# Optimization experiments

Hardware: AMD Instinct MI355X
Metric: run time of the kernel (lower is better)

## Reference

```python
import jax, jax.numpy as jnp
import numpy as np

N_HEAD = 16
HEAD_DIM = 64

def rotate_half(x):
    x1, x2 = jnp.split(x, 2, axis=-1)
    return jnp.concatenate((-x2, x1), axis=-1)

def rope_tables(T, dim):
    inv_freq = 1.0 / (10000.0 ** (jnp.arange(0, dim, 2, dtype=jnp.float32) / dim))
    t = jnp.arange(T, dtype=jnp.float32)
    freqs = jnp.einsum('i,j->ij', t, inv_freq)          # [T, dim/2]
    emb = jnp.concatenate((freqs, freqs), axis=-1)       # [T, dim]
    return jnp.cos(emb)[None, None], jnp.sin(emb)[None, None]  # [1,1,T,dim]

def setup_inputs() -> dict:
    key = jax.random.key(0)
    k1, k2, k3 = jax.random.split(key, 3)
    C = N_HEAD * HEAD_DIM
    x = jax.random.normal(k1, (2, 2048, C), dtype=jnp.float32)
    W_qkv = jax.random.normal(k2, (C, 3 * C), dtype=jnp.float32) * (1.0 / np.sqrt(C))
    W_proj = jax.random.normal(k3, (C, C), dtype=jnp.float32) * (1.0 / np.sqrt(C))
    return {"x": x, "W_qkv": W_qkv, "W_proj": W_proj}

def reference(x, W_qkv, W_proj):
    B, T, C = x.shape
    qkv = x @ W_qkv                                       # [B,T,3C]
    q, k, v = jnp.split(qkv, 3, axis=-1)
    def to_heads(a):
        return a.reshape(B, T, N_HEAD, HEAD_DIM).transpose(0, 2, 1, 3)  # [B,H,T,D]
    q, k, v = to_heads(q), to_heads(k), to_heads(v)
    cos, sin = rope_tables(T, HEAD_DIM)
    q = q * cos + rotate_half(q) * sin
    k = k * cos + rotate_half(k) * sin
    scale = 1.0 / jnp.sqrt(jnp.asarray(HEAD_DIM, dtype=x.dtype))
    scores = jnp.einsum('bhqd,bhkd->bhqk', q, k) * scale  # [B,H,T,T]
    causal = jnp.tril(jnp.ones((T, T), dtype=bool))
    scores = jnp.where(causal[None, None], scores, jnp.finfo(scores.dtype).min)
    attn = jax.nn.softmax(scores, axis=-1)
    out = jnp.einsum('bhqk,bhkd->bhqd', attn, v)          # [B,H,T,D]
    out = out.transpose(0, 2, 1, 3).reshape(B, T, C)
    return out @ W_proj
```

## Files before the change

### kernel.cpp

```cpp
#include <hip/hip_runtime.h>
#include <cstdint>
#include <cstddef>

typedef __attribute__((ext_vector_type(8))) short bf16x8;
typedef __attribute__((ext_vector_type(4))) float f32x4;

__device__ __forceinline__ unsigned short f2bf(float f) {
  unsigned int u = __builtin_bit_cast(unsigned int, f);
  u += 0x7FFFu + ((u >> 16) & 1u);
  return (unsigned short)(u >> 16);
}
__device__ __forceinline__ float bf2f(unsigned short h) {
  unsigned int u = ((unsigned int)h) << 16;
  return __builtin_bit_cast(float, u);
}

__device__ __forceinline__ void gl_lds16(const unsigned short* g, unsigned short* l) {
  __builtin_amdgcn_global_load_lds(
      (const __attribute__((address_space(1))) unsigned int*)(uintptr_t)g,
      (__attribute__((address_space(3))) unsigned int*)(unsigned int)(uintptr_t)l,
      16, 0, 0);
}

__global__ void k_prep(const float* __restrict__ x,
                       const float* __restrict__ Wqkv,
                       const float* __restrict__ Wproj,
                       unsigned short* __restrict__ xb,
                       unsigned short* __restrict__ wqt,
                       unsigned short* __restrict__ wpt,
                       float2* __restrict__ cstab) {
  __shared__ float tile[32][33];
  const int bid = blockIdx.x, tid = threadIdx.x;
  if (bid < 4096) {
    int i = bid * 256 + tid;
    float4 v = reinterpret_cast<const float4*>(x)[i];
    uint2 o;
    o.x = (unsigned int)f2bf(v.x) | ((unsigned int)f2bf(v.y) << 16);
    o.y = (unsigned int)f2bf(v.z) | ((unsigned int)f2bf(v.w) << 16);
    reinterpret_cast<uint2*>(xb)[i] = o;
  } else if (bid < 8192) {
    const float* in; unsigned short* out; int rows, cols, bx, by;
    if (bid < 7168) { in = Wqkv; out = wqt; rows = 1024; cols = 3072; bx = (bid - 4096) % 96; by = (bid - 4096) / 96; }
    else            { in = Wproj; out = wpt; rows = 1024; cols = 1024; bx = (bid - 7168) % 32; by = (bid - 7168) / 32; }
    int c0 = bx * 32, r0 = by * 32;
    int tx = tid & 31, ty = tid >> 5;
#pragma unroll
    for (int j = 0; j < 4; j++)
      tile[ty + j * 8][tx] = in[(size_t)(r0 + ty + j * 8) * cols + c0 + tx];
    __syncthreads();
#pragma unroll
    for (int j = 0; j < 4; j++)
      out[(size_t)(c0 + ty + j * 8) * rows + r0 + tx] = f2bf(tile[tx][ty + j * 8]);
  } else {
    int i = (bid - 8192) * 256 + tid;
    int t = i >> 5, j = i & 31;
    float invf = __powf(10000.0f, -(float)j / 32.0f);
    float ang = (float)t * invf;
    cstab[i] = make_float2(cosf(ang), sinf(ang));
  }
}

__global__ void k_gemm_qkv(const unsigned short* __restrict__ A,
                           const unsigned short* __restrict__ Bt,
                           const float2* __restrict__ cstab,
                           unsigned short* __restrict__ qh,
                           unsigned short* __restrict__ kh,
                           unsigned short* __restrict__ vt) {
  const int K = 1024;
  __shared__ unsigned short Ta[128 * 32];
  __shared__ unsigned short Tb[128 * 32];
  const int tid = threadIdx.x;
  const int bid0 = blockIdx.y * 24 + blockIdx.x;
  const int bid = (bid0 & 7) * 96 + (bid0 >> 3);
  const int m0 = (bid / 24) * 128, n0 = (bid % 24) * 128;
  const int w = tid >> 6, l = tid & 63;
  const int lr = l & 15, lg = l >> 4;
  const int wm = (w >> 1) * 64, wn = (w & 1) * 64;
  const int ssr = w * 32 + (l >> 2);
  const int ssc = (l & 3) * 8;
  unsigned short* ta0 = &Ta[w * 1024];
  unsigned short* tb0 = &Tb[w * 1024];
  f32x4 acc[4][4] = {};
  for (int k0 = 0; k0 < K; k0 += 32) {
    __syncthreads();
    gl_lds16(&A[(size_t)(m0 + ssr) * K + k0 + ssc],       ta0);
    gl_lds16(&A[(size_t)(m0 + ssr + 16) * K + k0 + ssc],  ta0 + 512);
    gl_lds16(&Bt[(size_t)(n0 + ssr) * K + k0 + ssc],      tb0);
    gl_lds16(&Bt[(size_t)(n0 + ssr + 16) * K + k0 + ssc], tb0 + 512);
    __syncthreads();
    bf16x8 af[4], bfr[4];
#pragma unroll
    for (int i = 0; i < 4; i++)
      af[i] = *(const bf16x8*)&Ta[(wm + i * 16 + lr) * 32 + lg * 8];
#pragma unroll
    for (int j = 0; j < 4; j++)
      bfr[j] = *(const bf16x8*)&Tb[(wn + j * 16 + lr) * 32 + lg * 8];
#pragma unroll
    for (int i = 0; i < 4; i++)
#pragma unroll
      for (int j = 0; j < 4; j++)
        acc[i][j] = __builtin_amdgcn_mfma_f32_16x16x32_bf16(af[i], bfr[j], acc[i][j], 0, 0, 0);
  }
  const int part = n0 >> 10;
  const int hbase = (n0 & 1023) + wn;
  if (part < 2) {
    unsigned short* dst = part ? kh : qh;
    const float scale = part ? 1.0f : 0.180336880111120420f;
#pragma unroll
    for (int i = 0; i < 4; i++) {
#pragma unroll
      for (int r = 0; r < 4; r++) {
        int gm = m0 + wm + i * 16 + lg * 4 + r;
        int t = gm & 2047, b = gm >> 11;
        float2 cs0 = cstab[t * 32 + lr];
        float2 cs1 = cstab[t * 32 + 16 + lr];
#pragma unroll
        for (int j = 0; j < 4; j++) {
          float val = acc[i][j][r];
          float par = acc[i][j ^ 2][r];
          float2 cs = (j & 1) ? cs1 : cs0;
          float out = (j < 2) ? (val * cs.x - par * cs.y)
                              : (val * cs.x + par * cs.y);
          int h = (hbase + j * 16) >> 6;
          int d = j * 16 + lr;
          int bh = b * 16 + h;
          dst[((size_t)(bh * 2048 + t)) * 64 + d] = f2bf(out * scale);
        }
      }
    }
  } else {
#pragma unroll
    for (int i = 0; i < 4; i++) {
      int tb = m0 + wm + i * 16 + lg * 4;
      int t0 = tb & 2047, b = tb >> 11;
#pragma unroll
      for (int j = 0; j < 4; j++) {
        int h = (hbase + j * 16) >> 6;
        int d = j * 16 + lr;
        int bh = b * 16 + h;
        unsigned short pv[4];
#pragma unroll
        for (int r = 0; r < 4; r++) pv[r] = f2bf(acc[i][j][r]);
        *(uint2*)&vt[((size_t)(bh * 64 + d)) * 2048 + t0] = *(uint2*)pv;
      }
    }
  }
}

__global__ void k_gemm_proj(const unsigned short* __restrict__ A,
                            const unsigned short* __restrict__ Bt,
                            float* __restrict__ C) {
  const int K = 1024;
  __shared__ unsigned short Ta[64 * 32];
  __shared__ unsigned short Tb[128 * 32];
  const int tid = threadIdx.x;
  const int bid0 = blockIdx.x;
  const int bid = (bid0 & 7) * 64 + (bid0 >> 3);
  const int n0 = (bid & 7) * 128;
  const int m0 = (bid >> 3) * 64;
  const int w = tid >> 6, l = tid & 63;
  const int lr = l & 15, lg = l >> 4;
  const int wn = w * 32;
  const int sra = tid >> 2, sca = (tid & 3) * 8;
  f32x4 acc[4][2] = {};
  for (int k0 = 0; k0 < K; k0 += 32) {
    __syncthreads();
    gl_lds16(&A[(size_t)(m0 + sra) * K + k0 + sca],        &Ta[tid * 8]);
    gl_lds16(&Bt[(size_t)(n0 + sra) * K + k0 + sca],       &Tb[tid * 8]);
    gl_lds16(&Bt[(size_t)(n0 + 64 + sra) * K + k0 + sca],  &Tb[(tid + 256) * 8]);
    __syncthreads();
    bf16x8 af[4], bfr[2];
#pragma unroll
    for (int i = 0; i < 4; i++)
      af[i] = *(const bf16x8*)&Ta[(i * 16 + lr) * 32 + lg * 8];
#pragma unroll
    for (int j = 0; j < 2; j++)
      bfr[j] = *(const bf16x8*)&Tb[(wn + j * 16 + lr) * 32 + lg * 8];
#pragma unroll
    for (int i = 0; i < 4; i++)
#pragma unroll
      for (int j = 0; j < 2; j++)
        acc[i][j] = __builtin_amdgcn_mfma_f32_16x16x32_bf16(af[i], bfr[j], acc[i][j], 0, 0, 0);
  }
#pragma unroll
  for (int i = 0; i < 4; i++)
#pragma unroll
    for (int j = 0; j < 2; j++)
#pragma unroll
      for (int r = 0; r < 4; r++)
        C[(size_t)(m0 + i * 16 + lg * 4 + r) * 1024 + n0 + wn + j * 16 + lr] = acc[i][j][r];
}

__global__ __launch_bounds__(256, 4) void k_attn(const unsigned short* __restrict__ qh,
                       const unsigned short* __restrict__ kh,
                       const unsigned short* __restrict__ vt,
                       unsigned short* __restrict__ att) {
  __shared__ unsigned short Kl[64 * 64];
  __shared__ unsigned short Vl[64 * 64];
  __shared__ unsigned short Pl[4][16 * 64];
  const int bid = blockIdx.x;
  const int xcd = bid & 7, u = bid >> 3;
  const int hl = u >> 5, v = u & 31;
  int qt;
  if      (hl == 0) qt = v;
  else if (hl == 1) qt = 31 - v;
  else if (hl == 2) qt = (v + 16) & 31;
  else              qt = (47 - v) & 31;
  const int bh = xcd * 4 + hl;
  const int b = bh >> 4, h = bh & 15;
  const int tid = threadIdx.x;
  const int w = tid >> 6, l = tid & 63;
  const int lr = l & 15, lg = l >> 4;
  const unsigned short* qbase = qh + (size_t)bh * 2048 * 64;
  const unsigned short* kbase = kh + (size_t)bh * 2048 * 64;
  const unsigned short* vbase = vt + (size_t)bh * 64 * 2048;
  char* KB = (char*)Kl;
  char* VB = (char*)Vl;
  char* PB = (char*)&Pl[w][0];
  const int swz = (lr & 7) << 4;
  const int sr = tid >> 2, sc = (tid & 3) * 16;
  const int sb0 = (sr * 128 + sc * 2) ^ ((sr & 7) << 4);
  const int sb1 = (sr * 128 + sc * 2 + 16) ^ ((sr & 7) << 4);

  const int q0 = qt * 64;
  const int qrow = q0 + w * 16 + lr;
  bf16x8 qa = *(const bf16x8*)&qbase[(size_t)qrow * 64 + lg * 8];
  bf16x8 qb = *(const bf16x8*)&qbase[(size_t)qrow * 64 + 32 + lg * 8];

  float mr = -3.0e38f, ls = 0.0f;
  f32x4 of[4] = {};
  uint4 ka0, ka1, va0, va1;

  auto issue = [&](int kv0) {
    const unsigned short* ksrc = &kbase[(size_t)(kv0 + sr) * 64 + sc];
    const unsigned short* vsrc = &vbase[(size_t)sr * 2048 + kv0 + sc];
    ka0 = *(const uint4*)ksrc; ka1 = *(const uint4*)(ksrc + 8);
    va0 = *(const uint4*)vsrc; va1 = *(const uint4*)(vsrc + 8);
  };

  issue(0);
  for (int kb = 0; kb <= qt; kb++) {
    const int kv0 = kb * 64;
    __syncthreads();
    *(uint4*)(KB + sb0) = ka0;  *(uint4*)(KB + sb1) = ka1;
    *(uint4*)(VB + sb0) = va0;  *(uint4*)(VB + sb1) = va1;
    __syncthreads();
    if (kb < qt) issue((kb + 1) * 64);

    f32x4 s[4] = {};
    __builtin_amdgcn_s_setprio(1);
#pragma unroll
    for (int kq = 0; kq < 4; kq++) {
      bf16x8 kf0 = *(const bf16x8*)(KB + (((kq * 16 + lr) * 128 + lg * 16) ^ swz));
      bf16x8 kf1 = *(const bf16x8*)(KB + (((kq * 16 + lr) * 128 + 64 + lg * 16) ^ swz));
      s[kq] = __builtin_amdgcn_mfma_f32_16x16x32_bf16(kf0, qa, s[kq], 0, 0, 0);
      s[kq] = __builtin_amdgcn_mfma_f32_16x16x32_bf16(kf1, qb, s[kq], 0, 0, 0);
    }
    __builtin_amdgcn_s_setprio(0);
    if (kb == qt) {
#pragma unroll
      for (int kq = 0; kq < 4; kq++)
#pragma unroll
        for (int r = 0; r < 4; r++)
          if (kv0 + kq * 16 + lg * 4 + r > qrow) s[kq][r] = -3.0e38f;
    }
    float pm = s[0][0];
#pragma unroll
    for (int kq = 0; kq < 4; kq++)
#pragma unroll
      for (int r = 0; r < 4; r++) pm = fmaxf(pm, s[kq][r]);
    pm = fmaxf(pm, __shfl_xor(pm, 16));
    pm = fmaxf(pm, __shfl_xor(pm, 32));
    float mnew = fmaxf(mr, pm);
    float alpha = __builtin_amdgcn_exp2f(mr - mnew);
    mr = mnew;
    float psum = 0.0f;
#pragma unroll
    for (int kq = 0; kq < 4; kq++)
#pragma unroll
      for (int r = 0; r < 4; r++) {
        float p = __builtin_amdgcn_exp2f(s[kq][r] - mnew);
        s[kq][r] = p;
        psum += p;
      }
    psum += __shfl_xor(psum, 16);
    psum += __shfl_xor(psum, 32);
    ls = ls * alpha + psum;
#pragma unroll
    for (int n = 0; n < 4; n++) {
      of[n][0] *= alpha; of[n][1] *= alpha; of[n][2] *= alpha; of[n][3] *= alpha;
    }
#pragma unroll
    for (int kq = 0; kq < 4; kq++) {
      uint2 pk;
      asm("v_cvt_pk_bf16_f32 %0, %1, %2" : "=v"(pk.x) : "v"(s[kq][0]), "v"(s[kq][1]));
      asm("v_cvt_pk_bf16_f32 %0, %1, %2" : "=v"(pk.y) : "v"(s[kq][2]), "v"(s[kq][3]));
      *(uint2*)(PB + ((lr * 128 + (kq * 16 + lg * 4) * 2) ^ swz)) = pk;
    }
    bf16x8 pb0 = *(const bf16x8*)(PB + ((lr * 128 + lg * 16) ^ swz));
    bf16x8 pb1 = *(const bf16x8*)(PB + ((lr * 128 + 64 + lg * 16) ^ swz));
    __builtin_amdgcn_s_setprio(1);
#pragma unroll
    for (int n = 0; n < 4; n++) {
      bf16x8 vf0 = *(const bf16x8*)(VB + (((n * 16 + lr) * 128 + lg * 16) ^ swz));
      bf16x8 vf1 = *(const bf16x8*)(VB + (((n * 16 + lr) * 128 + 64 + lg * 16) ^ swz));
      of[n] = __builtin_amdgcn_mfma_f32_16x16x32_bf16(vf0, pb0, of[n], 0, 0, 0);
      of[n] = __builtin_amdgcn_mfma_f32_16x16x32_bf16(vf1, pb1, of[n], 0, 0, 0);
    }
    __builtin_amdgcn_s_setprio(0);
  }

  float inv = 1.0f / ls;
#pragma unroll
  for (int n = 0; n < 4; n++) {
    uint2 pk;
    float o0 = of[n][0] * inv, o1 = of[n][1] * inv, o2 = of[n][2] * inv, o3 = of[n][3] * inv;
    asm("v_cvt_pk_bf16_f32 %0, %1, %2" : "=v"(pk.x) : "v"(o0), "v"(o1));
    asm("v_cvt_pk_bf16_f32 %0, %1, %2" : "=v"(pk.y) : "v"(o2), "v"(o3));
    *(uint2*)(PB + ((lr * 128 + (n * 16 + lg * 4) * 2) ^ swz)) = pk;
  }
  {
    int r2 = l >> 2, c2 = (l & 3) * 16;
    int bo0 = (r2 * 128 + c2 * 2) ^ ((r2 & 7) << 4);
    int bo1 = (r2 * 128 + c2 * 2 + 16) ^ ((r2 & 7) << 4);
    uint4 o0 = *(const uint4*)(PB + bo0);
    uint4 o1 = *(const uint4*)(PB + bo1);
    unsigned short* orow = att + (size_t)(b * 2048 + q0 + w * 16 + r2) * 1024 + h * 64 + c2;
    *(uint4*)orow = o0;
    *(uint4*)(orow + 8) = o1;
  }
}

extern "C" void kernel_launch(void* const* d_in, const int* in_sizes, int n_in,
                              void* d_out, int out_size, void* d_ws, size_t ws_size,
                              hipStream_t stream) {
  const float* x     = (const float*)d_in[0];
  const float* Wqkv  = (const float*)d_in[1];
  const float* Wproj = (const float*)d_in[2];
  float* out = (float*)d_out;

  char* ws = (char*)d_ws;
  size_t off = 0;
  auto alloc = [&](size_t bytes) { void* p = ws + off; off += (bytes + 255) & ~(size_t)255; return p; };
  unsigned short* xb   = (unsigned short*)alloc((size_t)4096 * 1024 * 2);
  unsigned short* wqt  = (unsigned short*)alloc((size_t)3072 * 1024 * 2);
  unsigned short* wpt  = (unsigned short*)alloc((size_t)1024 * 1024 * 2);
  unsigned short* qh   = (unsigned short*)alloc((size_t)32 * 2048 * 64 * 2);
  unsigned short* kh   = (unsigned short*)alloc((size_t)32 * 2048 * 64 * 2);
  unsigned short* vt   = (unsigned short*)alloc((size_t)32 * 64 * 2048 * 2);
  unsigned short* att  = (unsigned short*)alloc((size_t)4096 * 1024 * 2);
  float2* cstab = (float2*)alloc((size_t)2048 * 32 * 8);

  k_prep<<<8448, 256, 0, stream>>>(x, Wqkv, Wproj, xb, wqt, wpt, cstab);
  k_gemm_qkv<<<dim3(24, 32), 256, 0, stream>>>(xb, wqt, cstab, qh, kh, vt);
  k_attn<<<1024, 256, 0, stream>>>(qh, kh, vt, att);
  k_gemm_proj<<<512, 256, 0, stream>>>(att, wpt, out);
}
```

Measured before the change: 105.3 us.

## Multi-stage async LDS pipeline for QKV and projection GEMMs

```diff
diff --git a/kernel.cpp b/kernel.cpp
--- a/kernel.cpp
+++ b/kernel.cpp
@@ -60,15 +60,15 @@
   }
 }
 
-__global__ void k_gemm_qkv(const unsigned short* __restrict__ A,
+__global__ __launch_bounds__(256, 2) void k_gemm_qkv(const unsigned short* __restrict__ A,
                            const unsigned short* __restrict__ Bt,
                            const float2* __restrict__ cstab,
                            unsigned short* __restrict__ qh,
                            unsigned short* __restrict__ kh,
                            unsigned short* __restrict__ vt) {
   const int K = 1024;
-  __shared__ unsigned short Ta[128 * 32];
-  __shared__ unsigned short Tb[128 * 32];
+  __shared__ unsigned short Ta[4][128 * 32];
+  __shared__ unsigned short Tb[4][128 * 32];
   const int tid = threadIdx.x;
   const int bid0 = blockIdx.y * 24 + blockIdx.x;
   const int bid = (bid0 & 7) * 96 + (bid0 >> 3);
@@ -78,29 +78,49 @@
   const int wm = (w >> 1) * 64, wn = (w & 1) * 64;
   const int ssr = w * 32 + (l >> 2);
   const int ssc = (l & 3) * 8;
-  unsigned short* ta0 = &Ta[w * 1024];
-  unsigned short* tb0 = &Tb[w * 1024];
   f32x4 acc[4][4] = {};
-  for (int k0 = 0; k0 < K; k0 += 32) {
-    __syncthreads();
-    gl_lds16(&A[(size_t)(m0 + ssr) * K + k0 + ssc],       ta0);
-    gl_lds16(&A[(size_t)(m0 + ssr + 16) * K + k0 + ssc],  ta0 + 512);
+
+  auto stage = [&](int t) {
+    int buf = t & 3;
+    unsigned short* ta0 = &Ta[buf][w * 1024];
+    unsigned short* tb0 = &Tb[buf][w * 1024];
+    int k0 = t * 32;
+    gl_lds16(&A [(size_t)(m0 + ssr) * K + k0 + ssc],      ta0);
+    gl_lds16(&A [(size_t)(m0 + ssr + 16) * K + k0 + ssc], ta0 + 512);
     gl_lds16(&Bt[(size_t)(n0 + ssr) * K + k0 + ssc],      tb0);
     gl_lds16(&Bt[(size_t)(n0 + ssr + 16) * K + k0 + ssc], tb0 + 512);
-    __syncthreads();
+  };
+
+  stage(0); stage(1); stage(2);
+  asm volatile("s_waitcnt vmcnt(8)" ::: "memory");
+  asm volatile("s_barrier" ::: "memory");
+
+  for (int t = 0; t < 32; t++) {
+    if (t < 29) stage(t + 3);
+    const unsigned short* TA = &Ta[t & 3][0];
+    const unsigned short* TB = &Tb[t & 3][0];
     bf16x8 af[4], bfr[4];
 #pragma unroll
     for (int i = 0; i < 4; i++)
-      af[i] = *(const bf16x8*)&Ta[(wm + i * 16 + lr) * 32 + lg * 8];
+      af[i] = *(const bf16x8*)&TA[(wm + i * 16 + lr) * 32 + lg * 8];
 #pragma unroll
     for (int j = 0; j < 4; j++)
-      bfr[j] = *(const bf16x8*)&Tb[(wn + j * 16 + lr) * 32 + lg * 8];
+      bfr[j] = *(const bf16x8*)&TB[(wn + j * 16 + lr) * 32 + lg * 8];
+    __builtin_amdgcn_s_setprio(1);
 #pragma unroll
     for (int i = 0; i < 4; i++)
 #pragma unroll
       for (int j = 0; j < 4; j++)
         acc[i][j] = __builtin_amdgcn_mfma_f32_16x16x32_bf16(af[i], bfr[j], acc[i][j], 0, 0, 0);
-  }
+    __builtin_amdgcn_s_setprio(0);
+    if (t < 31) {
+      if (t < 29)       asm volatile("s_waitcnt vmcnt(8)" ::: "memory");
+      else if (t == 29) asm volatile("s_waitcnt vmcnt(4)" ::: "memory");
+      else              asm volatile("s_waitcnt vmcnt(0)" ::: "memory");
+      asm volatile("s_barrier" ::: "memory");
+    }
+  }
+
   const int part = n0 >> 10;
   const int hbase = (n0 & 1023) + wn;
   if (part < 2) {
@@ -147,12 +167,12 @@
   }
 }
 
-__global__ void k_gemm_proj(const unsigned short* __restrict__ A,
+__global__ __launch_bounds__(256, 3) void k_gemm_proj(const unsigned short* __restrict__ A,
                             const unsigned short* __restrict__ Bt,
                             float* __restrict__ C) {
   const int K = 1024;
-  __shared__ unsigned short Ta[64 * 32];
-  __shared__ unsigned short Tb[128 * 32];
+  __shared__ unsigned short Ta[4][64 * 32];
+  __shared__ unsigned short Tb[4][128 * 32];
   const int tid = threadIdx.x;
   const int bid0 = blockIdx.x;
   const int bid = (bid0 & 7) * 64 + (bid0 >> 3);
@@ -163,24 +183,43 @@
   const int wn = w * 32;
   const int sra = tid >> 2, sca = (tid & 3) * 8;
   f32x4 acc[4][2] = {};
-  for (int k0 = 0; k0 < K; k0 += 32) {
-    __syncthreads();
-    gl_lds16(&A[(size_t)(m0 + sra) * K + k0 + sca],        &Ta[tid * 8]);
-    gl_lds16(&Bt[(size_t)(n0 + sra) * K + k0 + sca],       &Tb[tid * 8]);
-    gl_lds16(&Bt[(size_t)(n0 + 64 + sra) * K + k0 + sca],  &Tb[(tid + 256) * 8]);
-    __syncthreads();
+
+  auto stage = [&](int t) {
+    int buf = t & 3;
+    int k0 = t * 32;
+    gl_lds16(&A[(size_t)(m0 + sra) * K + k0 + sca],        &Ta[buf][0] + tid * 8);
+    gl_lds16(&Bt[(size_t)(n0 + sra) * K + k0 + sca],       &Tb[buf][0] + tid * 8);
+    gl_lds16(&Bt[(size_t)(n0 + 64 + sra) * K + k0 + sca],  &Tb[buf][0] + (tid + 256) * 8);
+  };
+
+  stage(0); stage(1); stage(2);
+  asm volatile("s_waitcnt vmcnt(6)" ::: "memory");
+  asm volatile("s_barrier" ::: "memory");
+
+  for (int t = 0; t < 32; t++) {
+    if (t < 29) stage(t + 3);
+    const unsigned short* TA = &Ta[t & 3][0];
+    const unsigned short* TB = &Tb[t & 3][0];
     bf16x8 af[4], bfr[2];
 #pragma unroll
     for (int i = 0; i < 4; i++)
-      af[i] = *(const bf16x8*)&Ta[(i * 16 + lr) * 32 + lg * 8];
+      af[i] = *(const bf16x8*)&TA[(i * 16 + lr) * 32 + lg * 8];
 #pragma unroll
     for (int j = 0; j < 2; j++)
-      bfr[j] = *(const bf16x8*)&Tb[(wn + j * 16 + lr) * 32 + lg * 8];
+      bfr[j] = *(const bf16x8*)&TB[(wn + j * 16 + lr) * 32 + lg * 8];
+    __builtin_amdgcn_s_setprio(1);
 #pragma unroll
     for (int i = 0; i < 4; i++)
 #pragma unroll
       for (int j = 0; j < 2; j++)
         acc[i][j] = __builtin_amdgcn_mfma_f32_16x16x32_bf16(af[i], bfr[j], acc[i][j], 0, 0, 0);
+    __builtin_amdgcn_s_setprio(0);
+    if (t < 31) {
+      if (t < 29)       asm volatile("s_waitcnt vmcnt(6)" ::: "memory");
+      else if (t == 29) asm volatile("s_waitcnt vmcnt(3)" ::: "memory");
+      else              asm volatile("s_waitcnt vmcnt(0)" ::: "memory");
+      asm volatile("s_barrier" ::: "memory");
+    }
   }
 #pragma unroll
   for (int i = 0; i < 4; i++)
```

Result: slower. 108.1 us (+2.6%).
